# Kernel tuning notes

Measured on AMD Instinct MI355X. Metric: run time of the kernel, lower is better.

The kernel has to match this reference:

```python
import jax, jax.numpy as jnp
import numpy as np

NUM_USERS = 28000
NUM_ITEMS = 16000
N = NUM_USERS + NUM_ITEMS          # hash = row*N+col fits in int32 since N*N < 2**31
E = 8_000_000
KEEP_RATE = 0.5
SUB = 0.1
EXT = 0.5
RE_RATE = 0.8


def _gumbel_topk_sorted(key, weights, k):
    """Weighted sampling WITHOUT replacement of k edges (Gumbel top-k), sorted indices.
    Mirrors np.random.choice(..., replace=False, p=w/w.sum()); keep_index.sort()."""
    u = jax.random.uniform(key, weights.shape, minval=1e-12, maxval=1.0)
    scores = jnp.log(weights) - jnp.log(-jnp.log(u))
    _, idx = jax.lax.top_k(scores, k)
    return jnp.sort(idx)


def _degree_norm(rows, cols, n):
    """scipy pipeline: rowsum of ones-valued adj, d^-0.5 (inf->0), vals = d[row]*d[col].
    Note original uses ROW sums for both sides (d_mat_inv @ A @ d_mat_inv)."""
    deg = jax.ops.segment_sum(jnp.ones(rows.shape, jnp.float32), rows, num_segments=n)
    d_inv = jnp.where(deg > 0, jax.lax.rsqrt(deg), 0.0)
    return d_inv[rows] * d_inv[cols]


def _sub_adj(key, users, items, att, k):
    """create_sub_adj: weighted-sample k edges, add self loops, degree-normalize."""
    p = att / att.sum()
    keep = _gumbel_topk_sorted(key, p, k)
    loops = jnp.arange(N, dtype=users.dtype)
    rows = jnp.concatenate([loops, users[keep]])
    cols = jnp.concatenate([loops, items[keep]])
    return jnp.stack([rows, cols]), _degree_norm(rows, cols, N)


def setup_inputs() -> dict:
    key = jax.random.key(0)
    k1, k2, k3 = jax.random.split(key, 3)
    adj_rows = jax.random.randint(k1, (E,), 0, NUM_USERS, dtype=jnp.int32)              # user ids
    adj_cols = jax.random.randint(k2, (E,), 0, NUM_ITEMS, dtype=jnp.int32) + NUM_USERS  # item ids offset
    adj_values = jnp.ones((E,), jnp.float32)
    att_edge = jax.random.uniform(k3, (E,), jnp.float32, 0.0, 5.0)
    return {"adj_rows": adj_rows, "adj_cols": adj_cols, "adj_values": adj_values, "att_edge": att_edge}


def reference(adj_rows, adj_cols, adj_values, att_edge):
    key = jax.random.key(42)
    k_keep, k_er, k_ec, k_nr, k_nc, k_sub, k_cmp = jax.random.split(key, 7)

    # --- encoder adj: keep int(E*keepRate) edges, weights 1/exp(clip(att,3)+1e-8) ---
    att_clip = jnp.minimum(att_edge, 3.0)   # in-place att_f[att_f>3]=3 in the original
    w_keep = 1.0 / jnp.exp(att_clip + 1e-8)
    n_keep = int(E * KEEP_RATE)
    keep_idx = _gumbel_topk_sorted(k_keep, w_keep / w_keep.sum(), n_keep)

    loops = jnp.arange(N, dtype=adj_rows.dtype)
    rows = jnp.concatenate([loops, adj_rows[keep_idx]])   # [N + n_keep]
    cols = jnp.concatenate([loops, adj_cols[keep_idx]])
    enc_idx = jnp.stack([rows, cols])
    enc_vals = _degree_norm(rows, cols, N)

    # --- dropped edges (complement of keep_idx; exact count is static) ---
    keep_mask = jnp.zeros((E,), bool).at[keep_idx].set(True)
    n_drop = E - n_keep
    drop_idx = jnp.nonzero(~keep_mask, size=n_drop)[0]
    drop_rows, drop_cols = adj_rows[drop_idx], adj_cols[drop_idx]

    # --- extend + rewire: uniform choice WITH replacement ---
    n_ext = int(n_drop * EXT)
    ext_rows = rows[jax.random.randint(k_er, (n_ext,), 0, rows.shape[0])]
    ext_cols = cols[jax.random.randint(k_ec, (n_ext,), 0, cols.shape[0])]
    tmp_rows = jnp.concatenate([ext_rows, drop_rows])
    tmp_cols = jnp.concatenate([ext_cols, drop_cols])
    n_new = int(E * RE_RATE)
    new_rows = tmp_rows[jax.random.randint(k_nr, (n_new,), 0, tmp_rows.shape[0])]
    new_cols = tmp_cols[jax.random.randint(k_nc, (n_new,), 0, tmp_cols.shape[0])]

    # --- hash-based dedup -> decoder adj (ones values; padding rows get value 0) ---
    dec_rows = jnp.concatenate([new_rows, new_cols, loops, rows])
    dec_cols = jnp.concatenate([new_cols, new_rows, loops, cols])
    hash_val = dec_rows * N + dec_cols
    uniq = jnp.unique(hash_val, size=hash_val.shape[0], fill_value=-1)
    pad = uniq < 0
    ur = jnp.where(pad, 0, uniq // N)
    uc = jnp.where(pad, 0, uniq % N)
    dec_idx = jnp.stack([ur, uc])
    dec_vals = jnp.where(pad, 0.0, 1.0).astype(jnp.float32)

    # --- sub (flag=True: att+0.001) and cmp (flag=False: 1/exp(att+1e-8)) subgraphs ---
    n_sub = int(E * SUB)
    sub_idx, sub_vals = _sub_adj(k_sub, adj_rows, adj_cols, att_clip + 0.001, n_sub)
    cmp_idx, cmp_vals = _sub_adj(k_cmp, adj_rows, adj_cols, 1.0 / jnp.exp(att_clip + 1e-8), n_sub)

    return (enc_idx, enc_vals, dec_idx, dec_vals, sub_idx, sub_vals, cmp_idx, cmp_vals)
```

## Files before the change

### kernel.cpp

```cpp
#include <hip/hip_runtime.h>
#include <stdint.h>

#define PARTITIONABLE 1
#define SUM_LANES 8

#define E_EDGES   8000000
#define NVERT     44000
#define N_EXT     2000000
#define N_NEW     6400000
#define ROWS_LEN  4044000
#define SROWS_LEN 844000
#define DEC_LEN   16888000
#define BMP_WORDS 60500000
#define NSCB      59083
#define NBLK_E    1954
#define NSCB_B    231
#define NBLK_B    8

#define SPAN_EXT  4044000u
#define SPAN_NEW  6000000u

#define O0 0LL
#define O1 8088000LL
#define O2 12132000LL
#define O3 45908000LL
#define O4 62796000LL
#define O5 64484000LL
#define O6 65328000LL
#define O7 67016000LL
#define OUT_TOTAL 67860000

#define SC_SKEEP  0
#define SC_SSUB   1
#define SC_PREFIX 2
#define SC_KPRIME 3
#define SC_T      4
#define SC_M      5
#define SC_EQC    6
#define SC_EQN    7
#define SC_MUNIQ  8
#define SC_HIST   16
#define SC_PART   512

struct TF2 { uint32_t a, b; };

__host__ __device__ __forceinline__ TF2 tf2x32(uint32_t k0, uint32_t k1,
                                               uint32_t c0, uint32_t c1) {
  uint32_t ks2 = k0 ^ k1 ^ 0x1BD11BDAu;
  uint32_t x0 = c0 + k0, x1 = c1 + k1;
#define TFR(r) { x0 += x1; x1 = (x1 << (r)) | (x1 >> (32 - (r))); x1 ^= x0; }
  TFR(13) TFR(15) TFR(26) TFR(6)   x0 += k1;  x1 += ks2 + 1u;
  TFR(17) TFR(29) TFR(16) TFR(24)  x0 += ks2; x1 += k0 + 2u;
  TFR(13) TFR(15) TFR(26) TFR(6)   x0 += k0;  x1 += k1 + 3u;
  TFR(17) TFR(29) TFR(16) TFR(24)  x0 += k1;  x1 += ks2 + 4u;
  TFR(13) TFR(15) TFR(26) TFR(6)   x0 += ks2; x1 += k0 + 5u;
#undef TFR
  TF2 r; r.a = x0; r.b = x1; return r;
}

__device__ __forceinline__ uint32_t rbits(uint2 k, uint32_t i, uint32_t half) {
#if PARTITIONABLE
  TF2 r = tf2x32(k.x, k.y, 0u, i);
  return r.a ^ r.b;
#else
  if (i < half) return tf2x32(k.x, k.y, i, half + i).a;
  return tf2x32(k.x, k.y, i - half, i).b;
#endif
}

__device__ __forceinline__ uint32_t jrandint(uint2 k1, uint2 k2, uint32_t i,
                                             uint32_t half, uint32_t span) {
  uint32_t m1 = 65536u % span;
  uint32_t mult = (m1 * m1) % span;
  uint32_t hb = (mult != 0u) ? rbits(k1, i, half) : 0u;
  uint32_t lb = rbits(k2, i, half);
  uint32_t off = (hb % span) * mult + (lb % span);
  return off % span;
}

__device__ __forceinline__ float unif_from_bits(uint32_t bits) {
#pragma clang fp contract(off)
  float f = __uint_as_float((bits >> 9) | 0x3f800000u) - 1.0f;
  float u = f + 1e-12f;
  return fmaxf(1e-12f, u);
}

__device__ __forceinline__ float xla_logf(float x) {
#pragma clang fp contract(off)
  uint32_t bx = __float_as_uint(x);
  int emm0 = (int)(bx >> 23) - 127;
  float m = __uint_as_float((bx & 0x007fffffu) | 0x3f000000u);
  float e = 1.0f + (float)emm0;
  bool lt = (m < 0.707106781186547524f);
  float tmp1 = lt ? m : 0.0f;
  float t = m - 1.0f;
  e = e - (lt ? 1.0f : 0.0f);
  t = t + tmp1;
  float x2 = t * t;
  float x3 = x2 * t;
  float y, y1, y2;
  y  = t * 7.0376836292e-2f  + -1.1514610310e-1f;
  y1 = t * -1.2420140846e-1f +  1.4249322787e-1f;
  y2 = t * 2.0000714765e-1f  + -2.4999993993e-1f;
  y  = y  * t +  1.1676998740e-1f;
  y1 = y1 * t + -1.6668057665e-1f;
  y2 = y2 * t +  3.3333331174e-1f;
  y = y * x3 + y1;
  y = y * x3 + y2;
  y = y * x3;
  y1 = -2.12194440e-4f * e;
  float tmp2 = 0.5f * x2;
  y = y + y1;
  t = t - tmp2;
  y2 = 0.693359375f * e;
  t = t + y;
  t = t + y2;
  return t;
}

__device__ __forceinline__ float xla_expf(float x) {
#pragma clang fp contract(off)
  x = fminf(x, 88.3762626647950f);
  x = fmaxf(x, -88.3762626647949f);
  float fx = x * 1.44269504088896341f + 0.5f;
  float flr = floorf(fx);
  float t1 = flr * 0.693359375f;
  float t2 = flr * -2.12194440e-4f;
  x = x - t1;
  x = x - t2;
  float z = x * x;
  float y = 1.9875691500e-4f;
  y = y * x + 1.3981999507e-3f;
  y = y * x + 8.3334519073e-3f;
  y = y * x + 4.1665795894e-2f;
  y = y * x + 1.6666665459e-1f;
  y = y * x + 5.0000001201e-1f;
  y = y * z;
  y = y + x;
  y = y + 1.0f;
  int n = (int)flr;
  float p2n = __uint_as_float((uint32_t)(n + 127) << 23);
  return y * p2n;
}

__device__ __forceinline__ uint32_t score_key(float w, float S, float u) {
#pragma clang fp contract(off)
  float p = w / S;
  float lu = xla_logf(u);
  float g = xla_logf(-lu);
  float s = xla_logf(p) - g;
  uint32_t b = __float_as_uint(s);
  return (b & 0x80000000u) ? ~b : (b | 0x80000000u);
}

__global__ void zero_kernel(uint32_t* p, long long n) {
  long long i = (long long)blockIdx.x * blockDim.x + threadIdx.x;
  long long stride = (long long)gridDim.x * blockDim.x;
  for (; i < n; i += stride) p[i] = 0u;
}

__global__ void sentinel_kernel(float* outb, float code) {
  if (blockIdx.x == 0 && threadIdx.x == 0) outb[0] = code;
}

__global__ void w_kernel(const float* att, float* warr) {
#pragma clang fp contract(off)
  int i = blockIdx.x * 256 + threadIdx.x;
  if (i >= E_EDGES) return;
  float c = fminf(att[i], 3.0f);
  float x = c + 1e-8f;
  warr[i] = 1.0f / xla_expf(x);
}

#define SUMS_CH   16000
#define SUMS_V4   4000
#define PSTRIPE   2004
#define SUMS_B4   10
#define SUMS_NB   50
#define SUMS_NCH  500
#define SUMS_STG  448
__global__ __launch_bounds__(512) void sums_kernel(const float* warr, const float* att, float* scf) {
#pragma clang fp contract(off)
  __shared__ __align__(16) float buf0[8 * PSTRIPE];
  __shared__ __align__(16) float buf1[8 * PSTRIPE];
  __shared__ float lanes[SUM_LANES];
  int t = threadIdx.x;
  int which = blockIdx.x;
  const float4* src4 = (const float4*)(which == 0 ? warr : att);

  if (t >= 64) {
    for (int q = t - 64; q < SUMS_V4; q += SUMS_STG) {
      float4 v = src4[q];
      if (which == 1) {
        v.x = fminf(v.x, 3.0f) + 0.001f;
        v.y = fminf(v.y, 3.0f) + 0.001f;
        v.z = fminf(v.z, 3.0f) + 0.001f;
        v.w = fminf(v.w, 3.0f) + 0.001f;
      }
      int k = q >> 1;
      int s0 = (q & 1) * 4;
      buf0[(s0 + 0) * PSTRIPE + k] = v.x;
      buf0[(s0 + 1) * PSTRIPE + k] = v.y;
      buf0[(s0 + 2) * PSTRIPE + k] = v.z;
      buf0[(s0 + 3) * PSTRIPE + k] = v.w;
    }
  }
  __syncthreads();

  float acc = 0.0f;
  for (int c = 0; c < SUMS_NCH; ++c) {
    float* curb = (c & 1) ? buf1 : buf0;
    float* nxtb = (c & 1) ? buf0 : buf1;
    if (t >= 64) {
      if (c + 1 < SUMS_NCH) {
        const float4* base = src4 + (long long)(c + 1) * SUMS_V4;
        for (int q = t - 64; q < SUMS_V4; q += SUMS_STG) {
          float4 v = base[q];
          if (which == 1) {
            v.x = fminf(v.x, 3.0f) + 0.001f;
            v.y = fminf(v.y, 3.0f) + 0.001f;
            v.z = fminf(v.z, 3.0f) + 0.001f;
            v.w = fminf(v.w, 3.0f) + 0.001f;
          }
          int k = q >> 1;
          int s0 = (q & 1) * 4;
          nxtb[(s0 + 0) * PSTRIPE + k] = v.x;
          nxtb[(s0 + 1) * PSTRIPE + k] = v.y;
          nxtb[(s0 + 2) * PSTRIPE + k] = v.z;
          nxtb[(s0 + 3) * PSTRIPE + k] = v.w;
        }
      }
    } else if (t < SUM_LANES) {
      const float4* stripe4 = (const float4*)(curb + t * PSTRIPE);
      float4 ld[SUMS_B4];
#pragma unroll
      for (int u = 0; u < SUMS_B4; ++u) ld[u] = stripe4[u];
      for (int b = 0; b < SUMS_NB; ++b) {
        float4 nx[SUMS_B4];
        if (b + 1 < SUMS_NB) {
          int boff = (b + 1) * SUMS_B4;
#pragma unroll
          for (int u = 0; u < SUMS_B4; ++u) nx[u] = stripe4[boff + u];
        }
#pragma unroll
        for (int u = 0; u < SUMS_B4; ++u) {
          acc += ld[u].x; acc += ld[u].y; acc += ld[u].z; acc += ld[u].w;
        }
        if (b + 1 < SUMS_NB) {
#pragma unroll
          for (int u = 0; u < SUMS_B4; ++u) ld[u] = nx[u];
        }
      }
    }
    __syncthreads();
  }

  if (t < SUM_LANES) lanes[t] = acc;
  __syncthreads();
  if (t == 0) {
    float v[SUM_LANES];
    for (int q = 0; q < SUM_LANES; ++q) v[q] = lanes[q];
    int w = SUM_LANES;
    while (w > 1) { int h = w >> 1; for (int q = 0; q < h; ++q) v[q] = v[q] + v[q + h]; w = h; }
    scf[which] = v[0];
  }
}

__global__ void keys_kernel(const float* warr, const float* att, const float* scf,
                            uint32_t* keys, uint2 kk, int mode) {
  int i = blockIdx.x * 256 + threadIdx.x;
  if (i >= E_EDGES) return;
  float S = (mode == 1) ? scf[SC_SSUB] : scf[SC_SKEEP];
  float w;
  if (mode == 1) { float a = att[i]; w = fminf(a, 3.0f) + 0.001f; }
  else w = warr[i];
  uint32_t b = rbits(kk, (uint32_t)i, 4000000u);
  keys[i] = score_key(w, S, unif_from_bits(b));
}

__global__ void sel_reset_kernel(uint32_t* sc, uint32_t k) {
  int t = threadIdx.x;
  sc[SC_HIST + t] = 0u;
  if (t == 0) { sc[SC_PREFIX] = 0u; sc[SC_KPRIME] = k; sc[SC_EQC] = 0u; sc[SC_EQN] = 0u; }
}

__global__ void sel_hist_kernel(const uint32_t* keys, uint32_t* sc, int round) {
  __shared__ uint32_t h[256];
  int t = threadIdx.x;
  h[t] = 0u;
  __syncthreads();
  uint32_t pref = sc[SC_PREFIX];
  int shift = 24 - 8 * round;
  uint32_t maskHi = (round == 0) ? 0u : (0xFFFFFFFFu << (shift + 8));
  int i = blockIdx.x * 4096 + t;
#pragma unroll
  for (int it = 0; it < 16; ++it, i += 256) {
    if (i < E_EDGES) {
      uint32_t key = keys[i];
      if (((key ^ pref) & maskHi) == 0u) atomicAdd(&h[(key >> shift) & 0xffu], 1u);
    }
  }
  __syncthreads();
  if (h[t]) atomicAdd(&sc[SC_HIST + t], h[t]);
}

__global__ void sel_pick_kernel(uint32_t* sc, int round) {
  if (blockIdx.x != 0 || threadIdx.x != 0) return;
  uint32_t kprime = sc[SC_KPRIME];
  int shift = 24 - 8 * round;
  uint32_t cum = 0; uint32_t bsel = 0;
  for (int b = 255; b >= 0; --b) {
    uint32_t c = sc[SC_HIST + b];
    if (cum + c >= kprime) { bsel = (uint32_t)b; break; }
    cum += c;
  }
  sc[SC_PREFIX] |= bsel << shift;
  sc[SC_KPRIME] = kprime - cum;
  for (int b = 0; b < 256; ++b) sc[SC_HIST + b] = 0u;
  if (round == 3) { sc[SC_T] = sc[SC_PREFIX]; sc[SC_M] = sc[SC_KPRIME]; }
}

__global__ void eq_collect_kernel(const uint32_t* keys, uint32_t* sc, uint32_t* eql) {
  int i = blockIdx.x * 256 + threadIdx.x;
  if (i >= E_EDGES) return;
  if (keys[i] == sc[SC_T]) {
    uint32_t p = atomicAdd(&sc[SC_EQC], 1u);
    if (p < 4096u) eql[p] = (uint32_t)i;
  }
}

__global__ void eq_sort_kernel(uint32_t* sc, uint32_t* eql) {
  if (blockIdx.x != 0 || threadIdx.x != 0) return;
  uint32_t n = sc[SC_EQC]; if (n > 4096u) n = 4096u;
  sc[SC_EQN] = n;
  for (uint32_t a = 1; a < n; ++a) {
    uint32_t v = eql[a]; uint32_t b = a;
    while (b > 0 && eql[b - 1] > v) { eql[b] = eql[b - 1]; --b; }
    eql[b] = v;
  }
}

__device__ __forceinline__ int keep_flag(uint32_t key, uint32_t T, uint32_t m,
                                         const uint32_t* eql, uint32_t eqn, uint32_t i) {
  if (key > T) return 1;
  if (key != T) return 0;
  uint32_t lo = 0, hi = eqn;
  while (lo < hi) { uint32_t mid = (lo + hi) >> 1; if (eql[mid] < i) lo = mid + 1; else hi = mid; }
  return (lo < m) ? 1 : 0;
}

__global__ void cnt_flags_kernel(const uint32_t* keys, const uint32_t* sc,
                                 const uint32_t* eql, uint32_t* sblk) {
  __shared__ uint32_t s[256];
  int t = threadIdx.x;
  uint32_t T = sc[SC_T], m = sc[SC_M], eqn = sc[SC_EQN];
  int base = blockIdx.x * 4096 + t * 16;
  uint32_t cnt = 0;
#pragma unroll
  for (int j = 0; j < 16; ++j) {
    int i = base + j;
    if (i < E_EDGES) cnt += keep_flag(keys[i], T, m, eql, eqn, (uint32_t)i);
  }
  s[t] = cnt;
  __syncthreads();
  for (int off = 128; off > 0; off >>= 1) { if (t < off) s[t] += s[t + off]; __syncthreads(); }
  if (t == 0) sblk[blockIdx.x] = s[0];
}

__global__ void scan_small_kernel(uint32_t* a, int n, uint32_t* totalOut) {
  __shared__ uint32_t s[256];
  int t = threadIdx.x;
  uint32_t carry = 0;
  for (int base = 0; base < n; base += 256) {
    int idx = base + t;
    uint32_t v = (idx < n) ? a[idx] : 0u;
    s[t] = v;
    __syncthreads();
    for (int off = 1; off < 256; off <<= 1) {
      uint32_t x = 0; if (t >= off) x = s[t - off];
      __syncthreads();
      if (t >= off) s[t] += x;
      __syncthreads();
    }
    uint32_t incl = s[t];
    uint32_t tot = s[255];
    if (idx < n) a[idx] = incl - v + carry;
    carry += tot;
    __syncthreads();
  }
  if (t == 0 && totalOut) *totalOut = carry;
}

__global__ void hscan1_kernel(uint32_t* a, int n, uint32_t* part) {
  __shared__ uint32_t s[256];
  int t = threadIdx.x;
  int idx = blockIdx.x * 256 + t;
  uint32_t v = (idx < n) ? a[idx] : 0u;
  s[t] = v;
  __syncthreads();
  for (int off = 1; off < 256; off <<= 1) {
    uint32_t x = 0; if (t >= off) x = s[t - off];
    __syncthreads();
    if (t >= off) s[t] += x;
    __syncthreads();
  }
  if (idx < n) a[idx] = s[t] - v;
  if (t == 255) part[blockIdx.x] = s[255];
}

__global__ void hscan3_kernel(uint32_t* a, int n, const uint32_t* part) {
  int idx = blockIdx.x * 256 + threadIdx.x;
  if (idx < n) a[idx] += part[blockIdx.x];
}

__global__ void scatter_kernel(const uint32_t* keys, const uint32_t* sc, const uint32_t* eql,
                               const uint32_t* sblk, int* kidx, int* didx, int writeDrop) {
  __shared__ uint32_t s[256];
  int t = threadIdx.x;
  uint32_t T = sc[SC_T], m = sc[SC_M], eqn = sc[SC_EQN];
  int base = blockIdx.x * 4096 + t * 16;
  uint32_t fbits = 0, cnt = 0;
#pragma unroll
  for (int j = 0; j < 16; ++j) {
    int i = base + j; int f = 0;
    if (i < E_EDGES) f = keep_flag(keys[i], T, m, eql, eqn, (uint32_t)i);
    fbits |= ((uint32_t)f) << j; cnt += (uint32_t)f;
  }
  s[t] = cnt;
  __syncthreads();
  for (int off = 1; off < 256; off <<= 1) {
    uint32_t x = 0; if (t >= off) x = s[t - off];
    __syncthreads();
    if (t >= off) s[t] += x;
    __syncthreads();
  }
  uint32_t run = sblk[blockIdx.x] + (s[t] - cnt);
  for (int j = 0; j < 16; ++j) {
    int i = base + j;
    if (i >= E_EDGES) break;
    if ((fbits >> j) & 1u) {
      if (run < 4000000u) kidx[run] = i;
      run++;
    } else if (writeDrop) {
      uint32_t d = (uint32_t)i - run;
      if (d < 4000000u) didx[d] = i;
    }
  }
}

__global__ void build_rows_kernel(const int* kidx, const int* ar, const int* ac,
                                  int* rows, int* cols, int total) {
  int i = blockIdx.x * 256 + threadIdx.x;
  if (i >= total) return;
  if (i < NVERT) { rows[i] = i; cols[i] = i; }
  else {
    int j = kidx[i - NVERT];
    j = (j < 0) ? 0 : (j >= E_EDGES ? E_EDGES - 1 : j);
    rows[i] = ar[j]; cols[i] = ac[j];
  }
}

__global__ void deg_count_kernel(const int* rows, int* deg, int len) {
  int i = blockIdx.x * 256 + threadIdx.x;
  if (i >= len) return;
  int r = rows[i];
  r = (r < 0) ? 0 : (r >= NVERT ? NVERT - 1 : r);
  atomicAdd(&deg[r], 1);
}

__global__ void deg_inv_kernel(const int* deg, float* dinv) {
  int i = blockIdx.x * 256 + threadIdx.x;
  if (i >= NVERT) return;
  int d = deg[i];
  dinv[i] = (d > 0) ? (float)(1.0 / sqrt((double)d)) : 0.0f;
}

__global__ void graph_out_kernel(const int* rows, const int* cols, const float* dinv,
                                 float* outb, long long idxOff, long long valOff, int len) {
#pragma clang fp contract(off)
  int i = blockIdx.x * 256 + threadIdx.x;
  if (i >= len) return;
  int r = rows[i], c = cols[i];
  r = (r < 0) ? 0 : (r >= NVERT ? NVERT - 1 : r);
  c = (c < 0) ? 0 : (c >= NVERT ? NVERT - 1 : c);
  outb[idxOff + i] = (float)r;
  outb[idxOff + len + i] = (float)c;
  outb[valOff + i] = dinv[r] * dinv[c];
}

__global__ void newrc_kernel(const int* rows, const int* cols, const int* didx,
                             const int* ar, const int* ac, int* newr, int* newc,
                             uint2 knr1, uint2 knr2, uint2 knc1, uint2 knc2,
                             uint2 ker1, uint2 ker2, uint2 kec1, uint2 kec2) {
  int i = blockIdx.x * 256 + threadIdx.x;
  if (i >= N_NEW) return;
  uint32_t nr = jrandint(knr1, knr2, (uint32_t)i, 3200000u, SPAN_NEW);
  int v;
  if (nr < (uint32_t)N_EXT) {
    uint32_t e = jrandint(ker1, ker2, nr, 1000000u, SPAN_EXT);
    v = rows[e];
  } else {
    int d = didx[nr - (uint32_t)N_EXT];
    d = (d < 0) ? 0 : (d >= E_EDGES ? E_EDGES - 1 : d);
    v = ar[d];
  }
  newr[i] = v;
  uint32_t nc = jrandint(knc1, knc2, (uint32_t)i, 3200000u, SPAN_NEW);
  if (nc < (uint32_t)N_EXT) {
    uint32_t e = jrandint(kec1, kec2, nc, 1000000u, SPAN_EXT);
    v = cols[e];
  } else {
    int d = didx[nc - (uint32_t)N_EXT];
    d = (d < 0) ? 0 : (d >= E_EDGES ? E_EDGES - 1 : d);
    v = ac[d];
  }
  newc[i] = v;
}

__global__ void bmp_mark_kernel(const int* newr, const int* newc,
                                const int* rows, const int* cols, uint32_t* bmp) {
  int i = blockIdx.x * 256 + threadIdx.x;
  if (i >= DEC_LEN) return;
  int r, c;
  if (i < N_NEW) { r = newr[i]; c = newc[i]; }
  else if (i < 2 * N_NEW) { r = newc[i - N_NEW]; c = newr[i - N_NEW]; }
  else if (i < 2 * N_NEW + NVERT) { r = i - 2 * N_NEW; c = r; }
  else { int q = i - (2 * N_NEW + NVERT); r = rows[q]; c = cols[q]; }
  r = (r < 0) ? 0 : (r >= NVERT ? NVERT - 1 : r);
  c = (c < 0) ? 0 : (c >= NVERT ? NVERT - 1 : c);
  uint32_t h = (uint32_t)r * 44000u + (uint32_t)c;
  atomicOr(&bmp[h >> 5], 1u << (h & 31u));
}

__global__ void bmp_cnt_kernel(const uint32_t* bmp, uint32_t* blk) {
  __shared__ uint32_t s[256];
  int t = threadIdx.x;
  long long wbase = (long long)blockIdx.x * 1024 + (long long)t * 4;
  uint32_t c = 0;
#pragma unroll
  for (int j = 0; j < 4; ++j) {
    long long w = wbase + j;
    if (w < (long long)BMP_WORDS) c += __popc(bmp[w]);
  }
  s[t] = c;
  __syncthreads();
  for (int off = 128; off > 0; off >>= 1) { if (t < off) s[t] += s[t + off]; __syncthreads(); }
  if (t == 0) blk[blockIdx.x] = s[0];
}

__global__ void dec_out_kernel(const uint32_t* bmp, const uint32_t* blk, float* outb) {
  __shared__ uint32_t s[256];
  int t = threadIdx.x;
  long long wbase = (long long)blockIdx.x * 1024 + (long long)t * 4;
  uint32_t cn[4]; uint32_t tot = 0;
#pragma unroll
  for (int j = 0; j < 4; ++j) {
    long long w = wbase + j;
    cn[j] = (w < (long long)BMP_WORDS) ? (uint32_t)__popc(bmp[w]) : 0u;
    tot += cn[j];
  }
  s[t] = tot;
  __syncthreads();
  for (int off = 1; off < 256; off <<= 1) {
    uint32_t x = 0; if (t >= off) x = s[t - off];
    __syncthreads();
    if (t >= off) s[t] += x;
    __syncthreads();
  }
  uint32_t pos = blk[blockIdx.x] + (s[t] - tot);
  for (int j = 0; j < 4; ++j) {
    long long w = wbase + j;
    if (w >= (long long)BMP_WORDS) break;
    uint32_t word = bmp[w];
    while (word) {
      int b = __ffs(word) - 1;
      word &= word - 1u;
      uint32_t v = (uint32_t)w * 32u + (uint32_t)b;
      uint32_t ur = v / 44000u;
      uint32_t uc = v - ur * 44000u;
      if (pos < (uint32_t)DEC_LEN) {
        outb[O2 + pos] = (float)ur;
        outb[O2 + DEC_LEN + pos] = (float)uc;
        outb[O3 + pos] = 1.0f;
      }
      pos++;
    }
  }
}

__global__ void dec_pad_kernel(float* outb, const uint32_t* sc) {
  int p = blockIdx.x * 256 + threadIdx.x;
  if (p >= DEC_LEN) return;
  if ((uint32_t)p >= sc[SC_MUNIQ]) {
    outb[O2 + p] = 0.0f; outb[O2 + DEC_LEN + p] = 0.0f; outb[O3 + p] = 0.0f;
  }
}

static void jsplit2(uint2 k, uint2& k1, uint2& k2) {
#if PARTITIONABLE
  TF2 a = tf2x32(k.x, k.y, 0u, 0u), b = tf2x32(k.x, k.y, 0u, 1u);
  k1.x = a.a; k1.y = a.b; k2.x = b.a; k2.y = b.b;
#else
  TF2 a = tf2x32(k.x, k.y, 0u, 2u), b = tf2x32(k.x, k.y, 1u, 3u);
  k1.x = a.a; k1.y = b.a; k2.x = a.b; k2.y = b.b;
#endif
}

extern "C" void kernel_launch(void* const* d_in, const int* in_sizes, int n_in,
                              void* d_out, int out_size, void* d_ws, size_t ws_size,
                              hipStream_t stream) {
  float* outb = (float*)d_out;

  if (out_size != OUT_TOTAL) {
    sentinel_kernel<<<1, 64, 0, stream>>>(outb, 16777216.0f);
    return;
  }
  if (n_in < 4 || in_sizes[0] != E_EDGES || in_sizes[3] != E_EDGES) {
    sentinel_kernel<<<1, 64, 0, stream>>>(outb, 20971520.0f);
    return;
  }
  if (ws_size < 429300000ULL) {
    sentinel_kernel<<<1, 64, 0, stream>>>(outb, 25165824.0f);
    return;
  }

  const int* adj_rows = (const int*)d_in[0];
  const int* adj_cols = (const int*)d_in[1];
  const float* att = (const float*)d_in[3];
  char* ws = (char*)d_ws;

  uint32_t* KEYS  = (uint32_t*)(ws + 0LL);
  float*    WARR  = (float*)(ws + 32000000LL);
  int*      KIDX  = (int*)(ws + 64000000LL);
  int*      DIDX  = (int*)(ws + 80000000LL);
  int*      ROWS  = (int*)(ws + 96000000LL);
  int*      COLS  = (int*)(ws + 112176000LL);
  int*      NEWR  = (int*)(ws + 128352000LL);
  int*      NEWC  = (int*)(ws + 153952000LL);
  uint32_t* BMP   = (uint32_t*)(ws + 179552000LL);
  uint32_t* BLK   = (uint32_t*)(ws + 421552000LL);
  int*      DEG   = (int*)(ws + 421788544LL);
  float*    DINV  = (float*)(ws + 421964544LL);
  uint32_t* SBLK  = (uint32_t*)(ws + 422140544LL);
  uint32_t* SC    = (uint32_t*)(ws + 422148736LL);
  uint32_t* EQL   = (uint32_t*)(ws + 422152832LL);
  int*      CMPR  = (int*)(ws + 422169216LL);
  int*      CMPC  = (int*)(ws + 425545216LL);
  float*    DINVS = (float*)(ws + 428921216LL);
  float*    DINVC = (float*)(ws + 429097216LL);
  uint32_t* PART  = SC + SC_PART;

  TF2 K[7];
#if PARTITIONABLE
  for (int i = 0; i < 7; ++i) K[i] = tf2x32(0u, 42u, 0u, (uint32_t)i);
#else
  {
    TF2 T_[7];
    for (int i = 0; i < 7; ++i) T_[i] = tf2x32(0u, 42u, (uint32_t)i, (uint32_t)(7 + i));
    K[0].a = T_[0].a; K[0].b = T_[1].a;
    K[1].a = T_[2].a; K[1].b = T_[3].a;
    K[2].a = T_[4].a; K[2].b = T_[5].a;
    K[3].a = T_[6].a; K[3].b = T_[0].b;
    K[4].a = T_[1].b; K[4].b = T_[2].b;
    K[5].a = T_[3].b; K[5].b = T_[4].b;
    K[6].a = T_[5].b; K[6].b = T_[6].b;
  }
#endif
  uint2 kkeep, ker, kec, knr, knc, ksub, kcmp;
  kkeep.x = K[0].a; kkeep.y = K[0].b;
  ker.x = K[1].a; ker.y = K[1].b;
  kec.x = K[2].a; kec.y = K[2].b;
  knr.x = K[3].a; knr.y = K[3].b;
  knc.x = K[4].a; knc.y = K[4].b;
  ksub.x = K[5].a; ksub.y = K[5].b;
  kcmp.x = K[6].a; kcmp.y = K[6].b;
  uint2 ker1, ker2, kec1, kec2, knr1, knr2, knc1, knc2;
  jsplit2(ker, ker1, ker2); jsplit2(kec, kec1, kec2);
  jsplit2(knr, knr1, knr2); jsplit2(knc, knc1, knc2);

  zero_kernel<<<4096, 256, 0, stream>>>(BMP, (long long)BMP_WORDS);
  zero_kernel<<<1, 256, 0, stream>>>(SC, 1024LL);
  zero_kernel<<<2048, 256, 0, stream>>>((uint32_t*)KIDX, 8000000LL);
  w_kernel<<<31250, 256, 0, stream>>>(att, WARR);
  sums_kernel<<<2, 512, 0, stream>>>(WARR, att, (float*)SC);

  auto run_select = [&](uint32_t kcount) {
    sel_reset_kernel<<<1, 256, 0, stream>>>(SC, kcount);
    for (int r = 0; r < 4; ++r) {
      sel_hist_kernel<<<NBLK_E, 256, 0, stream>>>(KEYS, SC, r);
      sel_pick_kernel<<<1, 64, 0, stream>>>(SC, r);
    }
    eq_collect_kernel<<<31250, 256, 0, stream>>>(KEYS, SC, EQL);
    eq_sort_kernel<<<1, 64, 0, stream>>>(SC, EQL);
    cnt_flags_kernel<<<NBLK_E, 256, 0, stream>>>(KEYS, SC, EQL, SBLK);
    hscan1_kernel<<<NBLK_B, 256, 0, stream>>>(SBLK, NBLK_E, PART);
    scan_small_kernel<<<1, 256, 0, stream>>>(PART, NBLK_B, (uint32_t*)nullptr);
    hscan3_kernel<<<NBLK_B, 256, 0, stream>>>(SBLK, NBLK_E, PART);
  };

  keys_kernel<<<31250, 256, 0, stream>>>(WARR, att, (const float*)SC, KEYS, kkeep, 0);
  run_select(4000000u);
  scatter_kernel<<<NBLK_E, 256, 0, stream>>>(KEYS, SC, EQL, SBLK, KIDX, DIDX, 1);
  build_rows_kernel<<<15797, 256, 0, stream>>>(KIDX, adj_rows, adj_cols, ROWS, COLS, ROWS_LEN);
  zero_kernel<<<172, 256, 0, stream>>>((uint32_t*)DEG, (long long)NVERT);
  deg_count_kernel<<<15797, 256, 0, stream>>>(ROWS, DEG, ROWS_LEN);
  deg_inv_kernel<<<172, 256, 0, stream>>>(DEG, DINV);

  newrc_kernel<<<25000, 256, 0, stream>>>(ROWS, COLS, DIDX, adj_rows, adj_cols, NEWR, NEWC,
                                          knr1, knr2, knc1, knc2, ker1, ker2, kec1, kec2);
  bmp_mark_kernel<<<65969, 256, 0, stream>>>(NEWR, NEWC, ROWS, COLS, BMP);
  bmp_cnt_kernel<<<NSCB, 256, 0, stream>>>(BMP, BLK);
  hscan1_kernel<<<NSCB_B, 256, 0, stream>>>(BLK, NSCB, PART);
  scan_small_kernel<<<1, 256, 0, stream>>>(PART, NSCB_B, &SC[SC_MUNIQ]);
  hscan3_kernel<<<NSCB_B, 256, 0, stream>>>(BLK, NSCB, PART);

  keys_kernel<<<31250, 256, 0, stream>>>(WARR, att, (const float*)SC, KEYS, ksub, 1);
  run_select(800000u);
  scatter_kernel<<<NBLK_E, 256, 0, stream>>>(KEYS, SC, EQL, SBLK, KIDX, (int*)nullptr, 0);
  build_rows_kernel<<<3297, 256, 0, stream>>>(KIDX, adj_rows, adj_cols, NEWR, NEWC, SROWS_LEN);
  zero_kernel<<<172, 256, 0, stream>>>((uint32_t*)DEG, (long long)NVERT);
  deg_count_kernel<<<3297, 256, 0, stream>>>(NEWR, DEG, SROWS_LEN);
  deg_inv_kernel<<<172, 256, 0, stream>>>(DEG, DINVS);

  keys_kernel<<<31250, 256, 0, stream>>>(WARR, att, (const float*)SC, KEYS, kcmp, 2);
  run_select(800000u);
  scatter_kernel<<<NBLK_E, 256, 0, stream>>>(KEYS, SC, EQL, SBLK, KIDX, (int*)nullptr, 0);
  build_rows_kernel<<<3297, 256, 0, stream>>>(KIDX, adj_rows, adj_cols, CMPR, CMPC, SROWS_LEN);
  zero_kernel<<<172, 256, 0, stream>>>((uint32_t*)DEG, (long long)NVERT);
  deg_count_kernel<<<3297, 256, 0, stream>>>(CMPR, DEG, SROWS_LEN);
  deg_inv_kernel<<<172, 256, 0, stream>>>(DEG, DINVC);

  dec_out_kernel<<<NSCB, 256, 0, stream>>>(BMP, BLK, outb);
  dec_pad_kernel<<<65969, 256, 0, stream>>>(outb, SC);
  graph_out_kernel<<<3297, 256, 0, stream>>>(NEWR, NEWC, DINVS, outb, O4, O5, SROWS_LEN);
  graph_out_kernel<<<3297, 256, 0, stream>>>(CMPR, CMPC, DINVC, outb, O6, O7, SROWS_LEN);
  graph_out_kernel<<<15797, 256, 0, stream>>>(ROWS, COLS, DINV, outb, O0, O1, ROWS_LEN);
}
```

Before: 5.933 ms.

## Overlap sums with zeroing and precomputed Gumbel noise in one mega-kernel

Merges the two serial sum reductions, the bitmap and index zeroing, and a precomputation of the Gumbel noise log(-log(u)) for all three samplings into one launch. The idle device is filled while the two single-block reduction blocks run. The keys kernels then read the precomputed noise instead of recomputing threefry bits and two logs. The single-thread histogram pick is also replaced with a 256-thread parallel prefix scan. This costs an extra 96MB of workspace traffic and depends on the workspace being large enough, falling back to the old path otherwise.

```diff
diff --git a/kernel.cpp b/kernel.cpp
--- a/kernel.cpp
+++ b/kernel.cpp
@@ -41,6 +41,13 @@
 #define SC_MUNIQ  8
 #define SC_HIST   16
 #define SC_PART   512
+
+#define MB_SUMS   2
+#define MB_ZBMP   4096
+#define MB_ZKD    64
+#define MB_G      46875
+#define GUM_OFF   429306112LL
+#define WS_NEED_G 525306112ULL
 
 struct TF2 { uint32_t a, b; };
 
@@ -143,14 +150,18 @@
   return y * p2n;
 }
 
+__device__ __forceinline__ uint32_t orderkey(float s) {
+  uint32_t b = __float_as_uint(s);
+  return (b & 0x80000000u) ? ~b : (b | 0x80000000u);
+}
+
 __device__ __forceinline__ uint32_t score_key(float w, float S, float u) {
 #pragma clang fp contract(off)
   float p = w / S;
   float lu = xla_logf(u);
   float g = xla_logf(-lu);
   float s = xla_logf(p) - g;
-  uint32_t b = __float_as_uint(s);
-  return (b & 0x80000000u) ? ~b : (b | 0x80000000u);
+  return orderkey(s);
 }
 
 __global__ void zero_kernel(uint32_t* p, long long n) {
@@ -179,13 +190,39 @@
 #define SUMS_NB   50
 #define SUMS_NCH  500
 #define SUMS_STG  448
-__global__ __launch_bounds__(512) void sums_kernel(const float* warr, const float* att, float* scf) {
+__global__ __launch_bounds__(512) void phaseA_kernel(const float* warr, const float* att,
+                                                     float* scf, uint32_t* bmp,
+                                                     uint32_t* kdzero, float* gum,
+                                                     uint2 kkeep, uint2 ksub, uint2 kcmp) {
 #pragma clang fp contract(off)
   __shared__ __align__(16) float buf0[8 * PSTRIPE];
   __shared__ __align__(16) float buf1[8 * PSTRIPE];
   __shared__ float lanes[SUM_LANES];
   int t = threadIdx.x;
-  int which = blockIdx.x;
+  int blk = blockIdx.x;
+
+  if (blk >= MB_SUMS) {
+    if (blk < MB_SUMS + MB_ZBMP) {
+      int zid = (blk - MB_SUMS) * 512 + t;
+      for (long long w = zid; w < (long long)BMP_WORDS; w += (long long)MB_ZBMP * 512)
+        bmp[w] = 0u;
+    } else if (blk < MB_SUMS + MB_ZBMP + MB_ZKD) {
+      int zid = (blk - MB_SUMS - MB_ZBMP) * 512 + t;
+      for (long long w = zid; w < 8000000LL; w += (long long)MB_ZKD * 512)
+        kdzero[w] = 0u;
+    } else {
+      long long gi = (long long)(blk - MB_SUMS - MB_ZBMP - MB_ZKD) * 512 + t;
+      uint32_t set = (uint32_t)(gi / 8000000LL);
+      uint32_t i = (uint32_t)(gi - (long long)set * 8000000LL);
+      uint2 kk = (set == 0) ? kkeep : ((set == 1) ? ksub : kcmp);
+      uint32_t b = rbits(kk, i, 4000000u);
+      float u = unif_from_bits(b);
+      gum[gi] = xla_logf(-xla_logf(u));
+    }
+    return;
+  }
+
+  int which = blk;
   const float4* src4 = (const float4*)(which == 0 ? warr : att);
 
   if (t >= 64) {
@@ -267,15 +304,22 @@
 }
 
 __global__ void keys_kernel(const float* warr, const float* att, const float* scf,
-                            uint32_t* keys, uint2 kk, int mode) {
+                            uint32_t* keys, uint2 kk, int mode, const float* gum) {
+#pragma clang fp contract(off)
   int i = blockIdx.x * 256 + threadIdx.x;
   if (i >= E_EDGES) return;
   float S = (mode == 1) ? scf[SC_SSUB] : scf[SC_SKEEP];
   float w;
   if (mode == 1) { float a = att[i]; w = fminf(a, 3.0f) + 0.001f; }
   else w = warr[i];
-  uint32_t b = rbits(kk, (uint32_t)i, 4000000u);
-  keys[i] = score_key(w, S, unif_from_bits(b));
+  if (gum) {
+    float p = w / S;
+    float s = xla_logf(p) - gum[i];
+    keys[i] = orderkey(s);
+  } else {
+    uint32_t b = rbits(kk, (uint32_t)i, 4000000u);
+    keys[i] = score_key(w, S, unif_from_bits(b));
+  }
 }
 
 __global__ void sel_reset_kernel(uint32_t* sc, uint32_t k) {
@@ -305,19 +349,32 @@
 }
 
 __global__ void sel_pick_kernel(uint32_t* sc, int round) {
-  if (blockIdx.x != 0 || threadIdx.x != 0) return;
+  __shared__ uint32_t s[256];
+  int t = threadIdx.x;
   uint32_t kprime = sc[SC_KPRIME];
-  int shift = 24 - 8 * round;
-  uint32_t cum = 0; uint32_t bsel = 0;
-  for (int b = 255; b >= 0; --b) {
-    uint32_t c = sc[SC_HIST + b];
-    if (cum + c >= kprime) { bsel = (uint32_t)b; break; }
-    cum += c;
-  }
-  sc[SC_PREFIX] |= bsel << shift;
-  sc[SC_KPRIME] = kprime - cum;
-  for (int b = 0; b < 256; ++b) sc[SC_HIST + b] = 0u;
-  if (round == 3) { sc[SC_T] = sc[SC_PREFIX]; sc[SC_M] = sc[SC_KPRIME]; }
+  uint32_t rh = sc[SC_HIST + 255 - t];
+  s[t] = rh;
+  __syncthreads();
+  for (int off = 1; off < 256; off <<= 1) {
+    uint32_t x = 0; if (t >= off) x = s[t - off];
+    __syncthreads();
+    if (t >= off) s[t] += x;
+    __syncthreads();
+  }
+  uint32_t inc = s[t];
+  uint32_t prev = (t == 0) ? 0u : s[t - 1];
+  int win = (inc >= kprime) && (prev < kprime);
+  __syncthreads();
+  sc[SC_HIST + t] = 0u;
+  if (win) {
+    uint32_t bsel = (uint32_t)(255 - t);
+    int shift = 24 - 8 * round;
+    uint32_t newpref = sc[SC_PREFIX] | (bsel << shift);
+    sc[SC_PREFIX] = newpref;
+    uint32_t nk = kprime - prev;
+    sc[SC_KPRIME] = nk;
+    if (round == 3) { sc[SC_T] = newpref; sc[SC_M] = nk; }
+  }
 }
 
 __global__ void eq_collect_kernel(const uint32_t* keys, uint32_t* sc, uint32_t* eql) {
@@ -650,6 +707,12 @@
   float*    DINVC = (float*)(ws + 429097216LL);
   uint32_t* PART  = SC + SC_PART;
 
+  const int useG = (ws_size >= WS_NEED_G) ? 1 : 0;
+  float* GUM = useG ? (float*)(ws + GUM_OFF) : nullptr;
+  float* GUM_K = GUM;
+  float* GUM_S = useG ? GUM + 8000000 : nullptr;
+  float* GUM_C = useG ? GUM + 16000000 : nullptr;
+
   TF2 K[7];
 #if PARTITIONABLE
   for (int i = 0; i < 7; ++i) K[i] = tf2x32(0u, 42u, 0u, (uint32_t)i);
@@ -678,17 +741,18 @@
   jsplit2(ker, ker1, ker2); jsplit2(kec, kec1, kec2);
   jsplit2(knr, knr1, knr2); jsplit2(knc, knc1, knc2);
 
-  zero_kernel<<<4096, 256, 0, stream>>>(BMP, (long long)BMP_WORDS);
   zero_kernel<<<1, 256, 0, stream>>>(SC, 1024LL);
-  zero_kernel<<<2048, 256, 0, stream>>>((uint32_t*)KIDX, 8000000LL);
   w_kernel<<<31250, 256, 0, stream>>>(att, WARR);
-  sums_kernel<<<2, 512, 0, stream>>>(WARR, att, (float*)SC);
+  int megaBlocks = MB_SUMS + MB_ZBMP + MB_ZKD + (useG ? MB_G : 0);
+  phaseA_kernel<<<megaBlocks, 512, 0, stream>>>(WARR, att, (float*)SC, BMP,
+                                                (uint32_t*)KIDX, GUM,
+                                                kkeep, ksub, kcmp);
 
   auto run_select = [&](uint32_t kcount) {
     sel_reset_kernel<<<1, 256, 0, stream>>>(SC, kcount);
     for (int r = 0; r < 4; ++r) {
       sel_hist_kernel<<<NBLK_E, 256, 0, stream>>>(KEYS, SC, r);
-      sel_pick_kernel<<<1, 64, 0, stream>>>(SC, r);
+      sel_pick_kernel<<<1, 256, 0, stream>>>(SC, r);
     }
     eq_collect_kernel<<<31250, 256, 0, stream>>>(KEYS, SC, EQL);
     eq_sort_kernel<<<1, 64, 0, stream>>>(SC, EQL);
@@ -698,7 +762,7 @@
     hscan3_kernel<<<NBLK_B, 256, 0, stream>>>(SBLK, NBLK_E, PART);
   };
 
-  keys_kernel<<<31250, 256, 0, stream>>>(WARR, att, (const float*)SC, KEYS, kkeep, 0);
+  keys_kernel<<<31250, 256, 0, stream>>>(WARR, att, (const float*)SC, KEYS, kkeep, 0, GUM_K);
   run_select(4000000u);
   scatter_kernel<<<NBLK_E, 256, 0, stream>>>(KEYS, SC, EQL, SBLK, KIDX, DIDX, 1);
   build_rows_kernel<<<15797, 256, 0, stream>>>(KIDX, adj_rows, adj_cols, ROWS, COLS, ROWS_LEN);
@@ -714,7 +778,7 @@
   scan_small_kernel<<<1, 256, 0, stream>>>(PART, NSCB_B, &SC[SC_MUNIQ]);
   hscan3_kernel<<<NSCB_B, 256, 0, stream>>>(BLK, NSCB, PART);
 
-  keys_kernel<<<31250, 256, 0, stream>>>(WARR, att, (const float*)SC, KEYS, ksub, 1);
+  keys_kernel<<<31250, 256, 0, stream>>>(WARR, att, (const float*)SC, KEYS, ksub, 1, GUM_S);
   run_select(800000u);
   scatter_kernel<<<NBLK_E, 256, 0, stream>>>(KEYS, SC, EQL, SBLK, KIDX, (int*)nullptr, 0);
   build_rows_kernel<<<3297, 256, 0, stream>>>(KIDX, adj_rows, adj_cols, NEWR, NEWC, SROWS_LEN);
@@ -722,7 +786,7 @@
   deg_count_kernel<<<3297, 256, 0, stream>>>(NEWR, DEG, SROWS_LEN);
   deg_inv_kernel<<<172, 256, 0, stream>>>(DEG, DINVS);
 
-  keys_kernel<<<31250, 256, 0, stream>>>(WARR, att, (const float*)SC, KEYS, kcmp, 2);
+  keys_kernel<<<31250, 256, 0, stream>>>(WARR, att, (const float*)SC, KEYS, kcmp, 2, GUM_C);
   run_select(800000u);
   scatter_kernel<<<NBLK_E, 256, 0, stream>>>(KEYS, SC, EQL, SBLK, KIDX, (int*)nullptr, 0);
   build_rows_kernel<<<3297, 256, 0, stream>>>(KIDX, adj_rows, adj_cols, CMPR, CMPC, SROWS_LEN);
```

After: 5.639 ms. -4.9%, faster.
